# Kernel optimization log

Measured on AMD Instinct MI355X. Metric: run time of the kernel, lower is better.

## Reference

```python
import jax, jax.numpy as jnp
import numpy as np

B, N, K, D, H, FF, L, NH = 8, 50, 20, 3, 128, 2048, 3, 8
S = N * K
HD = H // NH


def setup_inputs() -> dict:
    key = jax.random.key(0)
    ks = jax.random.split(key, 16)
    visited = jax.random.uniform(ks[0], (B, S)) < 0.05
    # the single most-recent action per batch row (status flips 0 -> 1)
    action_idx = jax.random.randint(ks[1], (B,), 0, S)
    visited = visited.at[jnp.arange(B), action_idx].set(True)
    feats = jax.random.normal(ks[2], (B, S, D - 1)) * visited[:, :, None]
    state = jnp.concatenate([feats, visited[:, :, None].astype(jnp.float32)], axis=-1)
    prev_state = state.at[jnp.arange(B), action_idx, :].set(0.0)

    def w(k, shape, s=0.02):
        return jax.random.normal(k, shape, dtype=jnp.float32) * s

    return dict(
        prev_state=prev_state, state=state,
        W_pre=w(ks[3], (D, H)), b_pre=jnp.zeros(H),
        Wq=w(ks[4], (L, H, H)), bq=jnp.zeros((L, H)),
        Wk=w(ks[5], (L, H, H)), bk=jnp.zeros((L, H)),
        Wv=w(ks[6], (L, H, H)), bv=jnp.zeros((L, H)),
        Wo=w(ks[7], (L, H, H)), bo=jnp.zeros((L, H)),
        ln1_g=jnp.ones((L, H)), ln1_b=jnp.zeros((L, H)),
        Wff1=w(ks[8], (L, H, FF)), bff1=jnp.zeros((L, FF)),
        Wff2=w(ks[9], (L, FF, H)), bff2=jnp.zeros((L, H)),
        ln2_g=jnp.ones((L, H)), ln2_b=jnp.zeros((L, H)),
        W_comb=w(ks[10], (2 * H, H)), b_comb=jnp.zeros(H),
        W_dec=w(ks[11], (H, H)), b_dec=jnp.zeros(H),
        W_lin=w(ks[12], (S, S)), b_lin=jnp.zeros(S),
    )


def _layer_norm(x, g, b, eps=1e-5):
    m = jnp.mean(x, -1, keepdims=True)
    v = jnp.mean(jnp.square(x - m), -1, keepdims=True)
    return (x - m) * jax.lax.rsqrt(v + eps) * g + b


def _update_mask(state):
    # vectorized equivalent of the original Python-loop scatter mask
    status = state[:, :, -1] != 0                      # visited [B, S], S = K*N channel-major
    mask = status
    vis_kn = status.reshape(B, K, N)
    user_any = vis_kn.any(axis=1)                      # [B, N]: user visited on any channel
    mask = mask | jnp.broadcast_to(user_any[:, None, :], (B, K, N)).reshape(B, S)
    assigned = state.reshape(B, K, N, D).sum(-1) != 0  # [B, K, N]
    full = assigned.sum(-1) >= 2                       # [B, K]: channel already has 2 users
    mask = mask | jnp.broadcast_to(full[:, :, None], (B, K, N)).reshape(B, S)
    return mask


def reference(prev_state, state, W_pre, b_pre, Wq, bq, Wk, bk, Wv, bv, Wo, bo,
              ln1_g, ln1_b, Wff1, bff1, Wff2, bff2, ln2_g, ln2_b,
              W_comb, b_comb, W_dec, b_dec, W_lin, b_lin):
    mask = _update_mask(state)
    # exactly one status change per batch row (sequential RL step)
    diff = prev_state[:, :, -1] != state[:, :, -1]
    act_idx = jnp.argmax(diff, axis=1)                 # [B]

    x = state @ W_pre + b_pre                          # [B, S, H]
    scale = np.float32(1.0 / np.sqrt(HD))
    for i in range(L):  # 3 post-LN transformer encoder layers
        q = (x @ Wq[i] + bq[i]).reshape(B, S, NH, HD)
        k = (x @ Wk[i] + bk[i]).reshape(B, S, NH, HD)
        v = (x @ Wv[i] + bv[i]).reshape(B, S, NH, HD)
        att = jax.nn.softmax(jnp.einsum('bqhd,bkhd->bhqk', q, k) * scale, axis=-1)
        o = jnp.einsum('bhqk,bkhd->bqhd', att, v).reshape(B, S, H) @ Wo[i] + bo[i]
        x = _layer_norm(x + o, ln1_g[i], ln1_b[i])
        ff = jax.nn.relu(x @ Wff1[i] + bff1[i]) @ Wff2[i] + bff2[i]
        x = _layer_norm(x + ff, ln2_g[i], ln2_b[i])

    last = x[jnp.arange(B), act_idx]                   # [B, H]
    combined = jnp.concatenate([x.mean(axis=1), last], axis=-1)  # [B, 2H]
    g = combined @ W_comb + b_comb                     # [B, H]
    dec = x @ W_dec + b_dec                            # [B, S, H]
    scores = jnp.einsum('bsh,bh->bs', dec, g)          # [B, S]
    masked = scores @ W_lin + b_lin                    # Q-Learning head
    return jnp.where(mask, -jnp.inf, masked)
```

## Files before the change

### kernel.cpp

```cpp
#include <hip/hip_runtime.h>
#include <math.h>

#define Bb 8
#define Ss 1000
#define Kk 20
#define Nn 50
#define Dd 3
#define Hh 128
#define FFf 2048
#define Ll 3
#define NHh 8
#define HDd 16
#define ROWS (Bb*Ss)

#define SENTINEL -3.0e38f

typedef unsigned short ush;
typedef short short8 __attribute__((ext_vector_type(8)));
typedef float f32x4 __attribute__((ext_vector_type(4)));

__device__ __forceinline__ ush f2b(float f) {
  unsigned x = __float_as_uint(f);
  return (ush)((x + 0x7fff + ((x >> 16) & 1)) >> 16);
}

__global__ __launch_bounds__(256) void mask_kernel(const float* __restrict__ state,
                                                   const float* __restrict__ prev_state,
                                                   int* __restrict__ mask, int* __restrict__ act_idx) {
  int b = blockIdx.x, tid = threadIdx.x;
  __shared__ unsigned char status[Ss], assigned[Ss], uany[Nn], fullk[Kk];
  __shared__ int act;
  if (tid == 0) act = 1 << 30;
  __syncthreads();
  for (int s = tid; s < Ss; s += 256) {
    const float* st = state + ((size_t)b * Ss + s) * Dd;
    float f2 = st[2];
    status[s] = (f2 != 0.f);
    assigned[s] = ((st[0] + st[1] + f2) != 0.f);
    float p2 = prev_state[((size_t)b * Ss + s) * Dd + 2];
    if (p2 != f2) atomicMin(&act, s);
  }
  __syncthreads();
  if (tid < Nn) {
    unsigned char a = 0;
    for (int k = 0; k < Kk; ++k) a |= status[k * Nn + tid];
    uany[tid] = a;
  } else if (tid >= 64 && tid < 64 + Kk) {
    int k = tid - 64, cnt = 0;
    for (int n = 0; n < Nn; ++n) cnt += assigned[k * Nn + n];
    fullk[k] = (cnt >= 2);
  }
  __syncthreads();
  for (int s = tid; s < Ss; s += 256)
    mask[b * Ss + s] = (int)(status[s] | uany[s % Nn] | fullk[s / Nn]);
  if (tid == 0) act_idx[b] = (act >= Ss) ? 0 : act;
}

__global__ __launch_bounds__(256) void pre_kernel(const float* __restrict__ state,
                                                  const float* __restrict__ W_pre,
                                                  const float* __restrict__ b_pre,
                                                  float* __restrict__ x, ush* __restrict__ xbf) {
  int idx = blockIdx.x * 256 + threadIdx.x;
  if (idx >= ROWS * Hh) return;
  int row = idx >> 7, n = idx & 127;
  const float* st = state + (size_t)row * Dd;
  float v = b_pre[n] + st[0] * W_pre[n] + st[1] * W_pre[Hh + n] + st[2] * W_pre[2 * Hh + n];
  x[idx] = v;
  xbf[idx] = f2b(v);
}

#define S1 (384*128)
#define S2 (128*128)
#define S3 (2048*128)
#define S4 (128*2048)
#define SPL (S1+S2+S3+S4)
__global__ __launch_bounds__(256) void wprep_kernel(const float* __restrict__ Wq, const float* __restrict__ Wk,
                                                    const float* __restrict__ Wv, const float* __restrict__ Wo,
                                                    const float* __restrict__ Wff1, const float* __restrict__ Wff2,
                                                    const float* __restrict__ bq, const float* __restrict__ bk,
                                                    const float* __restrict__ bv,
                                                    ush* __restrict__ wqkvT, ush* __restrict__ woT,
                                                    ush* __restrict__ wff1T, ush* __restrict__ wff2T,
                                                    float* __restrict__ bqkv) {
  int idx = blockIdx.x * 256 + threadIdx.x;
  if (idx < Ll * SPL) {
    int l = idx / SPL, r = idx % SPL;
    if (r < S1) {
      int k = r / 384, n = r % 384;
      float v = (n < 128) ? Wq[((size_t)l * Hh + k) * Hh + n]
              : (n < 256) ? Wk[((size_t)l * Hh + k) * Hh + (n - 128)]
                          : Wv[((size_t)l * Hh + k) * Hh + (n - 256)];
      wqkvT[((size_t)l * 384 + n) * 128 + k] = f2b(v);
    } else if (r < S1 + S2) {
      int rr = r - S1; int k = rr >> 7, n = rr & 127;
      woT[((size_t)l * 128 + n) * 128 + k] = f2b(Wo[((size_t)l * Hh + k) * Hh + n]);
    } else if (r < S1 + S2 + S3) {
      int rr = r - S1 - S2; int k = rr >> 11, n = rr & 2047;
      wff1T[((size_t)l * 2048 + n) * 128 + k] = f2b(Wff1[((size_t)l * Hh + k) * FFf + n]);
    } else {
      int rr = r - S1 - S2 - S3; int k = rr >> 7, n = rr & 127;
      wff2T[((size_t)l * 128 + n) * 2048 + k] = f2b(Wff2[((size_t)l * FFf + k) * Hh + n]);
    }
  }
  if (idx < Ll * 384) {
    int l = idx / 384, c = idx % 384;
    bqkv[idx] = (c < 128) ? bq[l * Hh + c] : (c < 256 ? bk[l * Hh + c - 128] : bv[l * Hh + c - 256]);
  }
}

#define LDP 40
template <int ABF16, int OBF16, int RELU, int PARTIAL, int QKVV>
__global__ __launch_bounds__(256) void gemm_mfma(const void* __restrict__ A, const ush* __restrict__ Wt,
                                                 const float* __restrict__ bias, void* __restrict__ out,
                                                 int M, int N, int K, int klen, ush* __restrict__ vTout) {
  __shared__ ush As[64 * LDP];
  __shared__ ush Bs[64 * LDP];
  int tid = threadIdx.x;
  int lane = tid & 63, wid = tid >> 6;
  int wr = wid >> 1, wc = wid & 1;
  int m0 = blockIdx.y * 64, n0 = blockIdx.x * 64;
  int lrow = tid >> 2, lk = (tid & 3) << 3;
  int quad = lane >> 4, l16 = lane & 15, kb = quad << 3;
  int kstart = PARTIAL ? blockIdx.z * klen : 0;

  f32x4 acc[2][2];
#pragma unroll
  for (int i = 0; i < 2; ++i)
#pragma unroll
    for (int j = 0; j < 2; ++j) acc[i][j] = (f32x4){0.f, 0.f, 0.f, 0.f};

  for (int k0 = kstart; k0 < kstart + klen; k0 += 32) {
    if (ABF16) {
      short8 av = *(const short8*)((const ush*)A + (size_t)(m0 + lrow) * K + k0 + lk);
      *(short8*)&As[lrow * LDP + lk] = av;
    } else {
      const float* ap = (const float*)A + (size_t)(m0 + lrow) * K + k0 + lk;
      short8 s;
#pragma unroll
      for (int i = 0; i < 8; ++i) s[i] = (short)f2b(ap[i]);
      *(short8*)&As[lrow * LDP + lk] = s;
    }
    short8 bv = *(const short8*)&Wt[(size_t)(n0 + lrow) * K + k0 + lk];
    *(short8*)&Bs[lrow * LDP + lk] = bv;
    __syncthreads();

    short8 a0 = *(short8*)&As[(wr * 32 + l16) * LDP + kb];
    short8 a1 = *(short8*)&As[(wr * 32 + 16 + l16) * LDP + kb];
    short8 b0 = *(short8*)&Bs[(wc * 32 + l16) * LDP + kb];
    short8 b1 = *(short8*)&Bs[(wc * 32 + 16 + l16) * LDP + kb];
    acc[0][0] = __builtin_amdgcn_mfma_f32_16x16x32_bf16(a0, b0, acc[0][0], 0, 0, 0);
    acc[0][1] = __builtin_amdgcn_mfma_f32_16x16x32_bf16(a0, b1, acc[0][1], 0, 0, 0);
    acc[1][0] = __builtin_amdgcn_mfma_f32_16x16x32_bf16(a1, b0, acc[1][0], 0, 0, 0);
    acc[1][1] = __builtin_amdgcn_mfma_f32_16x16x32_bf16(a1, b1, acc[1][1], 0, 0, 0);
    __syncthreads();
  }

  float* pout = PARTIAL ? ((float*)out + (size_t)blockIdx.z * M * N) : (float*)out;
#pragma unroll
  for (int i = 0; i < 2; ++i)
#pragma unroll
    for (int j = 0; j < 2; ++j) {
      int col = n0 + wc * 32 + j * 16 + l16;
      int rbase = m0 + wr * 32 + i * 16 + quad * 4;
      float bval = (!PARTIAL || blockIdx.z == 0) ? bias[col] : 0.f;
#pragma unroll
      for (int v = 0; v < 4; ++v) {
        float o = acc[i][j][v] + bval;
        if (RELU) o = fmaxf(o, 0.f);
        if (QKVV && col >= 256) {
          int row = rbase + v;
          int bb2 = row / 1000, qq = row - bb2 * 1000;
          vTout[((size_t)(bb2 * 128 + (col - 256))) * 1024 + qq] = f2b(o);
        } else if (OBF16) {
          ((ush*)out)[(size_t)(rbase + v) * N + col] = f2b(o);
        } else {
          pout[(size_t)(rbase + v) * N + col] = o;
        }
      }
    }
}

#define WLP 132
__global__ __launch_bounds__(256) void wo_ln_kernel(const ush* __restrict__ A, const ush* __restrict__ Wt,
                                                    const float* __restrict__ bias,
                                                    const float* __restrict__ ln_g, const float* __restrict__ ln_b,
                                                    float* __restrict__ x, ush* __restrict__ xbf) {
  __shared__ char smem[64 * WLP * 4];
  ush* As = (ush*)smem;
  ush* Bs = As + 64 * LDP;
  float* xs = (float*)smem;
  __shared__ float pbias[128], pg[128], pb2[128];

  int tid = threadIdx.x, lane = tid & 63, w = tid >> 6;
  int l16 = lane & 15, quad = lane >> 4, kb = quad * 8;
  int m0 = blockIdx.x * 64;
  if (tid < 128) { pbias[tid] = bias[tid]; pg[tid] = ln_g[tid]; pb2[tid] = ln_b[tid]; }

  f32x4 acc[8];
#pragma unroll
  for (int j = 0; j < 8; ++j) acc[j] = (f32x4){0.f, 0.f, 0.f, 0.f};

  int srow = tid >> 2, slk = (tid & 3) << 3;
  for (int k0 = 0; k0 < 128; k0 += 32) {
    *(short8*)&As[srow * LDP + slk] = *(const short8*)(A + (size_t)(m0 + srow) * 128 + k0 + slk);
#pragma unroll
    for (int rr = 0; rr < 2; ++rr) {
      int row = rr * 64 + srow;
      *(short8*)&Bs[row * LDP + slk] = *(const short8*)(Wt + (size_t)row * 128 + k0 + slk);
    }
    __syncthreads();
    short8 aA = *(short8*)&As[(w * 16 + l16) * LDP + kb];
#pragma unroll
    for (int j = 0; j < 8; ++j) {
      short8 bj = *(short8*)&Bs[(j * 16 + l16) * LDP + kb];
      acc[j] = __builtin_amdgcn_mfma_f32_16x16x32_bf16(aA, bj, acc[j], 0, 0, 0);
    }
    __syncthreads();
  }

  for (int e = tid; e < 64 * 32; e += 256) {
    int idx = e * 4; int row = idx >> 7, col = idx & 127;
    *(float4*)&xs[row * WLP + col] = *(const float4*)&x[(size_t)(m0 + row) * 128 + col];
  }
  __syncthreads();

  float v[8][4], s1[4] = {0.f, 0.f, 0.f, 0.f}, s2[4] = {0.f, 0.f, 0.f, 0.f};
#pragma unroll
  for (int j = 0; j < 8; ++j) {
    int col = j * 16 + l16;
#pragma unroll
    for (int r = 0; r < 4; ++r) {
      int rowt = w * 16 + quad * 4 + r;
      float vv = acc[j][r] + pbias[col] + xs[rowt * WLP + col];
      v[j][r] = vv; s1[r] += vv; s2[r] += vv * vv;
    }
  }
#pragma unroll
  for (int m = 1; m <= 8; m <<= 1) {
#pragma unroll
    for (int r = 0; r < 4; ++r) { s1[r] += __shfl_xor(s1[r], m); s2[r] += __shfl_xor(s2[r], m); }
  }
#pragma unroll
  for (int r = 0; r < 4; ++r) {
    int rowt = w * 16 + quad * 4 + r;
    float mean = s1[r] * (1.f / 128.f);
    float var = s2[r] * (1.f / 128.f) - mean * mean;
    float rstd = rsqrtf(var + 1e-5f);
#pragma unroll
    for (int j = 0; j < 8; ++j) {
      int col = j * 16 + l16;
      float o = (v[j][r] - mean) * rstd * pg[col] + pb2[col];
      size_t gi = (size_t)(m0 + rowt) * 128 + col;
      x[gi] = o; xbf[gi] = f2b(o);
    }
  }
}

#define F2P 72
__global__ __launch_bounds__(256) void ff2_ln_kernel(const ush* __restrict__ A,
                                                     const ush* __restrict__ Wt,
                                                     const float* __restrict__ bias,
                                                     const float* __restrict__ ln_g, const float* __restrict__ ln_b,
                                                     float* __restrict__ x, ush* __restrict__ xbf) {
  __shared__ ush As[32 * F2P];
  __shared__ ush Bs[128 * F2P];
  __shared__ float red1[2][2][16], red2[2][2][16];
  __shared__ float pbias[128], pg[128], pb[128];

  int tid = threadIdx.x, lane = tid & 63, w = tid >> 6;
  int wr = w & 1, wc = w >> 1;
  int l16 = lane & 15, quad = lane >> 4, kb = quad * 8;
  int m0 = blockIdx.x * 32;
  if (tid < 128) { pbias[tid] = bias[tid]; pg[tid] = ln_g[tid]; pb[tid] = ln_b[tid]; }

  f32x4 acc[4];
#pragma unroll
  for (int j = 0; j < 4; ++j) acc[j] = (f32x4){0.f, 0.f, 0.f, 0.f};

  int arow = tid >> 3, alk = (tid & 7) << 3;
  const ush* Ap = A + (size_t)(m0 + arow) * 2048 + alk;

  short8 pa = *(const short8*)Ap;
  short8 pbr[4];
#pragma unroll
  for (int rep = 0; rep < 4; ++rep) {
    int idx = rep * 256 + tid;
    int row = idx >> 3, lk = (idx & 7) << 3;
    pbr[rep] = *(const short8*)(Wt + (size_t)row * 2048 + lk);
  }

  for (int k0 = 0; k0 < 2048; k0 += 64) {
    *(short8*)&As[arow * F2P + alk] = pa;
#pragma unroll
    for (int rep = 0; rep < 4; ++rep) {
      int idx = rep * 256 + tid;
      int row = idx >> 3, lk = (idx & 7) << 3;
      *(short8*)&Bs[row * F2P + lk] = pbr[rep];
    }
    __syncthreads();
    if (k0 + 64 < 2048) {
      pa = *(const short8*)(Ap + k0 + 64);
#pragma unroll
      for (int rep = 0; rep < 4; ++rep) {
        int idx = rep * 256 + tid;
        int row = idx >> 3, lk = (idx & 7) << 3;
        pbr[rep] = *(const short8*)(Wt + (size_t)row * 2048 + k0 + 64 + lk);
      }
    }
#pragma unroll
    for (int kk = 0; kk < 2; ++kk) {
      short8 a = *(short8*)&As[(wr * 16 + l16) * F2P + kk * 32 + kb];
#pragma unroll
      for (int j = 0; j < 4; ++j) {
        short8 b = *(short8*)&Bs[(wc * 64 + j * 16 + l16) * F2P + kk * 32 + kb];
        acc[j] = __builtin_amdgcn_mfma_f32_16x16x32_bf16(a, b, acc[j], 0, 0, 0);
      }
    }
    __syncthreads();
  }

  float v[4][4], s1[4] = {0.f, 0.f, 0.f, 0.f}, s2[4] = {0.f, 0.f, 0.f, 0.f};
#pragma unroll
  for (int j = 0; j < 4; ++j) {
    int col = wc * 64 + j * 16 + l16;
#pragma unroll
    for (int r = 0; r < 4; ++r) {
      int row = m0 + wr * 16 + quad * 4 + r;
      float vv = acc[j][r] + pbias[col] + x[(size_t)row * Hh + col];
      v[j][r] = vv; s1[r] += vv; s2[r] += vv * vv;
    }
  }
#pragma unroll
  for (int m = 1; m <= 8; m <<= 1) {
#pragma unroll
    for (int r = 0; r < 4; ++r) { s1[r] += __shfl_xor(s1[r], m); s2[r] += __shfl_xor(s2[r], m); }
  }
  if (l16 == 0) {
#pragma unroll
    for (int r = 0; r < 4; ++r) {
      red1[wr][wc][quad * 4 + r] = s1[r];
      red2[wr][wc][quad * 4 + r] = s2[r];
    }
  }
  __syncthreads();
#pragma unroll
  for (int r = 0; r < 4; ++r) {
    int qr = quad * 4 + r;
    float t1 = red1[wr][0][qr] + red1[wr][1][qr];
    float t2 = red2[wr][0][qr] + red2[wr][1][qr];
    float mean = t1 * (1.f / 128.f);
    float var = t2 * (1.f / 128.f) - mean * mean;
    float rstd = rsqrtf(var + 1e-5f);
    int row = m0 + wr * 16 + quad * 4 + r;
#pragma unroll
    for (int j = 0; j < 4; ++j) {
      int col = wc * 64 + j * 16 + l16;
      float o = (v[j][r] - mean) * rstd * pg[col] + pb[col];
      size_t gi = (size_t)row * Hh + col;
      x[gi] = o; xbf[gi] = f2b(o);
    }
  }
}

__global__ __launch_bounds__(256) void attn_mfma(const ush* __restrict__ qkv,
                                                 const ush* __restrict__ vT,
                                                 ush* __restrict__ attn_o) {
  int blk = blockIdx.x;
  int local = blk >> 3;
  int bh = ((blk & 7) << 3) | (local >> 4);
  int qt = local & 15;
  int b = bh >> 3, h = bh & 7;
  int qbase = qt * 64;
  int tid = threadIdx.x, lane = tid & 63, w = tid >> 6;
  int l16 = lane & 15, quad = lane >> 4, kb = quad * 8;

  __shared__ ush Ks[2][64][40];
  __shared__ ush Vs[2][16][72];
  __shared__ ush Pb[4][16][72];

  if (tid < 128) {
    int row = tid >> 1, g = tid & 1;
    *(short8*)&Ks[0][row][16 + g * 8] = (short8){0, 0, 0, 0, 0, 0, 0, 0};
    *(short8*)&Ks[1][row][16 + g * 8] = (short8){0, 0, 0, 0, 0, 0, 0, 0};
  }

  int qrow = qbase + w * 16 + l16; if (qrow >= Ss) qrow = Ss - 1;
  short8 aq = *(const short8*)(qkv + (size_t)(b * Ss + qrow) * 384 + h * HDd + kb);

  int srow = tid >> 1, sg = tid & 1;
  int sd = (tid - 128) >> 3, skg = (tid - 128) & 7;
  const ush* kbase = qkv + (size_t)b * Ss * 384 + 128 + h * HDd;
  const ush* vbase = vT + (size_t)(b * 128 + h * 16) * 1024;

  if (tid < 128) {
    short8 s8 = (short8){0, 0, 0, 0, 0, 0, 0, 0};
    if (srow < Ss) s8 = *(const short8*)(kbase + (size_t)srow * 384 + sg * 8);
    *(short8*)&Ks[0][srow][sg * 8] = s8;
  } else {
    *(short8*)&Vs[0][sd][skg * 8] = *(const short8*)(vbase + (size_t)sd * 1024 + skg * 8);
  }
  __syncthreads();

  const short one_b = (short)0x3F80;
  const short8 ones = (short8){one_b, one_b, one_b, one_b, one_b, one_b, one_b, one_b};
  f32x4 acc_pv = (f32x4){0.f, 0.f, 0.f, 0.f};
  f32x4 acc_l = (f32x4){0.f, 0.f, 0.f, 0.f};
  const f32x4 zero4 = (f32x4){0.f, 0.f, 0.f, 0.f};

  for (int it = 0; it < 16; ++it) {
    int k0 = it * 64;
    int cur = it & 1, nxt = cur ^ 1;
    bool have = (it + 1 < 16);

    short8 gk, gv;
    if (have) {
      if (tid < 128) {
        gk = (short8){0, 0, 0, 0, 0, 0, 0, 0};
        int key = k0 + 64 + srow;
        if (key < Ss) gk = *(const short8*)(kbase + (size_t)key * 384 + sg * 8);
      } else {
        gv = *(const short8*)(vbase + (size_t)sd * 1024 + k0 + 64 + skg * 8);
      }
    }

    bool tail = (k0 + 64 > Ss);
#pragma unroll
    for (int kn = 0; kn < 4; ++kn) {
      short8 ak = *(short8*)&Ks[cur][kn * 16 + l16][kb];
      f32x4 s = __builtin_amdgcn_mfma_f32_16x16x32_bf16(ak, aq, zero4, 0, 0, 0);
      float p0 = __expf(s[0] * 0.25f);
      float p1 = __expf(s[1] * 0.25f);
      float p2 = __expf(s[2] * 0.25f);
      float p3 = __expf(s[3] * 0.25f);
      if (tail) {
        int keyb = k0 + kn * 16 + quad * 4;
        if (keyb + 0 >= Ss) p0 = 0.f;
        if (keyb + 1 >= Ss) p1 = 0.f;
        if (keyb + 2 >= Ss) p2 = 0.f;
        if (keyb + 3 >= Ss) p3 = 0.f;
      }
      unsigned lo, hi;
      asm("v_cvt_pk_bf16_f32 %0, %1, %2" : "=v"(lo) : "v"(p0), "v"(p1));
      asm("v_cvt_pk_bf16_f32 %0, %1, %2" : "=v"(hi) : "v"(p2), "v"(p3));
      *(uint2*)&Pb[w][l16][kn * 16 + quad * 4] = make_uint2(lo, hi);
    }

    short8 pa0 = *(short8*)&Pb[w][l16][kb];
    short8 pa1 = *(short8*)&Pb[w][l16][32 + kb];
    short8 vb0 = *(short8*)&Vs[cur][l16][kb];
    short8 vb1 = *(short8*)&Vs[cur][l16][32 + kb];
    acc_pv = __builtin_amdgcn_mfma_f32_16x16x32_bf16(pa0, vb0, acc_pv, 0, 0, 0);
    acc_pv = __builtin_amdgcn_mfma_f32_16x16x32_bf16(pa1, vb1, acc_pv, 0, 0, 0);
    acc_l = __builtin_amdgcn_mfma_f32_16x16x32_bf16(pa0, ones, acc_l, 0, 0, 0);
    acc_l = __builtin_amdgcn_mfma_f32_16x16x32_bf16(pa1, ones, acc_l, 0, 0, 0);

    if (have) {
      if (tid < 128) *(short8*)&Ks[nxt][srow][sg * 8] = gk;
      else *(short8*)&Vs[nxt][sd][skg * 8] = gv;
    }
    __syncthreads();
  }

#pragma unroll
  for (int r = 0; r < 4; ++r) {
    int q = qbase + w * 16 + quad * 4 + r;
    if (q < Ss)
      attn_o[((size_t)(b * Ss + q)) * Hh + h * HDd + l16] = f2b(acc_pv[r] / acc_l[r]);
  }
}

__global__ __launch_bounds__(128) void mean_part_kernel(const float* __restrict__ x,
                                                        float* __restrict__ mpart) {
  int c = blockIdx.x, b = blockIdx.y, n = threadIdx.x;
  const float* xb = x + ((size_t)b * Ss + c * 125) * Hh + n;
  float s = 0.f;
#pragma unroll 5
  for (int i = 0; i < 125; ++i) s += xb[(size_t)i * Hh];
  mpart[(c * Bb + b) * Hh + n] = s;
}

__global__ __launch_bounds__(128) void ghc_kernel(const float* __restrict__ x, const float* __restrict__ mpart,
                                                  const int* __restrict__ act_idx,
                                                  const float* __restrict__ W_comb, const float* __restrict__ b_comb,
                                                  const float* __restrict__ W_dec, const float* __restrict__ b_dec,
                                                  float* __restrict__ h, float* __restrict__ cb) {
  int b = blockIdx.x, n = threadIdx.x;
  __shared__ float cs[2 * Hh], gs[Hh], red[2];
  float mean = 0.f;
#pragma unroll
  for (int c = 0; c < 8; ++c) mean += mpart[(c * Bb + b) * Hh + n];
  cs[n] = mean * (1.f / Ss);
  cs[Hh + n] = x[((size_t)b * Ss + act_idx[b]) * Hh + n];
  __syncthreads();
  float acc = b_comb[n];
  for (int j = 0; j < 2 * Hh; ++j) acc += cs[j] * W_comb[(size_t)j * Hh + n];
  gs[n] = acc;
  __syncthreads();
  float hv = 0.f;
  for (int c = 0; c < Hh; ++c) hv += W_dec[(size_t)n * Hh + c] * gs[c];
  h[b * Hh + n] = hv;
  float t = b_dec[n] * gs[n];
  for (int off = 32; off; off >>= 1) t += __shfl_down(t, off);
  if ((n & 63) == 0) red[n >> 6] = t;
  __syncthreads();
  if (n == 0) cb[b] = red[0] + red[1];
}

__global__ __launch_bounds__(256) void scores_kernel(const float* __restrict__ x, const float* __restrict__ h,
                                                     const float* __restrict__ cb, float* __restrict__ scores) {
  int wid = threadIdx.x >> 6, lane = threadIdx.x & 63;
  int row = blockIdx.x * 4 + wid;
  if (row >= ROWS) return;
  int b = row / Ss;
  const float* xr = x + (size_t)row * Hh;
  const float* hb = h + b * Hh;
  float s = xr[lane] * hb[lane] + xr[lane + 64] * hb[lane + 64];
  for (int off = 32; off; off >>= 1) s += __shfl_down(s, off);
  if (lane == 0) scores[row] = s + cb[b];
}

__global__ __launch_bounds__(256) void final_part(const float* __restrict__ scores,
                                                  const float* __restrict__ W_lin,
                                                  float* __restrict__ fpart) {
  int spc = blockIdx.x, kc = blockIdx.y;
  int tid = threadIdx.x;
  __shared__ float ss[8][125];
  for (int i = tid; i < 8 * 125; i += 256) {
    int bb = i / 125, s = i - bb * 125;
    ss[bb][s] = scores[bb * Ss + kc * 125 + s];
  }
  __syncthreads();
  if (tid < 250) {
    int sp = spc * 250 + tid;
    float acc[8];
#pragma unroll
    for (int bb = 0; bb < 8; ++bb) acc[bb] = 0.f;
    const float* wl = &W_lin[(size_t)(kc * 125) * Ss + sp];
#pragma unroll 5
    for (int s = 0; s < 125; ++s) {
      float wv = wl[(size_t)s * Ss];
#pragma unroll
      for (int bb = 0; bb < 8; ++bb) acc[bb] = fmaf(ss[bb][s], wv, acc[bb]);
    }
#pragma unroll
    for (int bb = 0; bb < 8; ++bb)
      fpart[((size_t)kc * Bb + bb) * Ss + sp] = acc[bb];
  }
}

__global__ __launch_bounds__(256) void final_combine(const float* __restrict__ fpart,
                                                     const float* __restrict__ b_lin,
                                                     const int* __restrict__ mask,
                                                     float* __restrict__ out) {
  int b = blockIdx.y;
  int sp = blockIdx.x * 256 + threadIdx.x;
  if (sp >= Ss) return;
  float acc = b_lin[sp];
#pragma unroll
  for (int kc = 0; kc < 8; ++kc) acc += fpart[((size_t)kc * Bb + b) * Ss + sp];
  out[b * Ss + sp] = mask[b * Ss + sp] ? SENTINEL : acc;
}

extern "C" void kernel_launch(void* const* d_in, const int* in_sizes, int n_in,
                              void* d_out, int out_size, void* d_ws, size_t ws_size,
                              hipStream_t stream) {
  const float* prev_state = (const float*)d_in[0];
  const float* state = (const float*)d_in[1];
  const float* W_pre = (const float*)d_in[2];
  const float* b_pre = (const float*)d_in[3];
  const float* Wq = (const float*)d_in[4];
  const float* bq = (const float*)d_in[5];
  const float* Wk = (const float*)d_in[6];
  const float* bk = (const float*)d_in[7];
  const float* Wv = (const float*)d_in[8];
  const float* bv = (const float*)d_in[9];
  const float* Wo = (const float*)d_in[10];
  const float* bo = (const float*)d_in[11];
  const float* ln1_g = (const float*)d_in[12];
  const float* ln1_b = (const float*)d_in[13];
  const float* Wff1 = (const float*)d_in[14];
  const float* bff1 = (const float*)d_in[15];
  const float* Wff2 = (const float*)d_in[16];
  const float* bff2 = (const float*)d_in[17];
  const float* ln2_g = (const float*)d_in[18];
  const float* ln2_b = (const float*)d_in[19];
  const float* W_comb = (const float*)d_in[20];
  const float* b_comb = (const float*)d_in[21];
  const float* W_dec = (const float*)d_in[22];
  const float* b_dec = (const float*)d_in[23];
  const float* W_lin = (const float*)d_in[24];
  const float* b_lin = (const float*)d_in[25];

  char* wsp = (char*)d_ws;
  auto alloc = [&](size_t bytes) { char* p = wsp; wsp += (bytes + 255) & ~(size_t)255; return p; };
  int* mask = (int*)alloc(ROWS * 4);
  int* act = (int*)alloc(Bb * 4);
  ush* wqkvT = (ush*)alloc((size_t)Ll * 384 * 128 * 2);
  ush* woT = (ush*)alloc((size_t)Ll * 128 * 128 * 2);
  ush* wff1T = (ush*)alloc((size_t)Ll * 2048 * 128 * 2);
  ush* wff2T = (ush*)alloc((size_t)Ll * 128 * 2048 * 2);
  float* bqkv = (float*)alloc((size_t)Ll * 384 * 4);
  float* x = (float*)alloc((size_t)ROWS * Hh * 4);
  ush* xbf = (ush*)alloc((size_t)ROWS * Hh * 2);
  ush* qkv_bf = (ush*)alloc((size_t)ROWS * 384 * 2);
  ush* vT = (ush*)alloc((size_t)Bb * 128 * 1024 * 2);
  ush* attn_ob = (ush*)alloc((size_t)ROWS * Hh * 2);
  float* mpart = (float*)alloc((size_t)8 * Bb * Hh * 4);
  float* hbuf = (float*)alloc((size_t)Bb * Hh * 4);
  float* cb = (float*)alloc((size_t)Bb * 4);
  float* scores = (float*)alloc((size_t)ROWS * 4);
  float* fpart = (float*)alloc((size_t)8 * Bb * Ss * 4);
  ush* ffb = (ush*)alloc((size_t)ROWS * FFf * 2);

  wprep_kernel<<<dim3((Ll * SPL + 255) / 256), 256, 0, stream>>>(Wq, Wk, Wv, Wo, Wff1, Wff2, bq, bk, bv,
                                                                 wqkvT, woT, wff1T, wff2T, bqkv);
  mask_kernel<<<Bb, 256, 0, stream>>>(state, prev_state, mask, act);
  pre_kernel<<<dim3((ROWS * Hh + 255) / 256), 256, 0, stream>>>(state, W_pre, b_pre, x, xbf);

  for (int l = 0; l < Ll; ++l) {
    gemm_mfma<1, 1, 0, 0, 1><<<dim3(384 / 64, ROWS / 64), 256, 0, stream>>>(
        xbf, wqkvT + (size_t)l * 384 * 128, bqkv + l * 384, qkv_bf, ROWS, 384, 128, 128, vT);
    attn_mfma<<<dim3(1024), 256, 0, stream>>>(qkv_bf, vT, attn_ob);
    wo_ln_kernel<<<dim3(ROWS / 64), 256, 0, stream>>>(
        attn_ob, woT + (size_t)l * 128 * 128, bo + l * Hh, ln1_g + l * Hh, ln1_b + l * Hh, x, xbf);
    gemm_mfma<1, 1, 1, 0, 0><<<dim3(2048 / 64, ROWS / 64), 256, 0, stream>>>(
        xbf, wff1T + (size_t)l * 2048 * 128, bff1 + l * FFf, ffb, ROWS, 2048, 128, 128, nullptr);
    ff2_ln_kernel<<<dim3(ROWS / 32), 256, 0, stream>>>(
        ffb, wff2T + (size_t)l * 128 * 2048, bff2 + l * Hh, ln2_g + l * Hh, ln2_b + l * Hh, x, xbf);
  }

  mean_part_kernel<<<dim3(8, Bb), 128, 0, stream>>>(x, mpart);
  ghc_kernel<<<Bb, 128, 0, stream>>>(x, mpart, act, W_comb, b_comb, W_dec, b_dec, hbuf, cb);
  scores_kernel<<<dim3(ROWS / 4), 256, 0, stream>>>(x, hbuf, cb, scores);
  final_part<<<dim3(4, 8), 256, 0, stream>>>(scores, W_lin, fpart);
  final_combine<<<dim3(4, Bb), 256, 0, stream>>>(fpart, b_lin, mask, (float*)d_out);
}
```

Baseline: 385.6 us.

## Double-buffer LDS in GEMM kernels and unify Wo/FF2 LayerNorm GEMMs

The generic MFMA GEMM now uses two LDS buffers, prefetching the next K-tile into registers during the MFMA work and storing it to the other buffer, which removes one barrier per iteration. The separate Wo+LN kernel is replaced by a templated version of the FF2+LN kernel (32-row tiles, double-buffered) that also serves K=128, giving more blocks for the Wo projection. W_dec is transposed during weight prep so the ghc kernel reads it coalesced. The costs are twice the LDS per block, which may limit occupancy, and a Wo path that now shares the FF2 kernel's tile shape.

```diff
diff --git a/kernel.cpp b/kernel.cpp
--- a/kernel.cpp
+++ b/kernel.cpp
@@ -78,10 +78,10 @@
                                                     const float* __restrict__ Wv, const float* __restrict__ Wo,
                                                     const float* __restrict__ Wff1, const float* __restrict__ Wff2,
                                                     const float* __restrict__ bq, const float* __restrict__ bk,
-                                                    const float* __restrict__ bv,
+                                                    const float* __restrict__ bv, const float* __restrict__ W_dec,
                                                     ush* __restrict__ wqkvT, ush* __restrict__ woT,
                                                     ush* __restrict__ wff1T, ush* __restrict__ wff2T,
-                                                    float* __restrict__ bqkv) {
+                                                    float* __restrict__ bqkv, float* __restrict__ wdecT) {
   int idx = blockIdx.x * 256 + threadIdx.x;
   if (idx < Ll * SPL) {
     int l = idx / SPL, r = idx % SPL;
@@ -106,22 +106,28 @@
     int l = idx / 384, c = idx % 384;
     bqkv[idx] = (c < 128) ? bq[l * Hh + c] : (c < 256 ? bk[l * Hh + c - 128] : bv[l * Hh + c - 256]);
   }
+  if (idx < Hh * Hh) {
+    int k = idx >> 7, n = idx & 127;
+    wdecT[(size_t)n * Hh + k] = W_dec[idx];
+  }
 }
 
 #define LDP 40
-template <int ABF16, int OBF16, int RELU, int PARTIAL, int QKVV>
-__global__ __launch_bounds__(256) void gemm_mfma(const void* __restrict__ A, const ush* __restrict__ Wt,
-                                                 const float* __restrict__ bias, void* __restrict__ out,
-                                                 int M, int N, int K, int klen, ush* __restrict__ vTout) {
-  __shared__ ush As[64 * LDP];
-  __shared__ ush Bs[64 * LDP];
+template <int RELU, int QKVV>
+__global__ __launch_bounds__(256) void gemm_mfma(const ush* __restrict__ A, const ush* __restrict__ Wt,
+                                                 const float* __restrict__ bias, ush* __restrict__ out,
+                                                 int N, int K, ush* __restrict__ vTout) {
+  __shared__ ush As[2][64 * LDP];
+  __shared__ ush Bs[2][64 * LDP];
   int tid = threadIdx.x;
   int lane = tid & 63, wid = tid >> 6;
   int wr = wid >> 1, wc = wid & 1;
   int m0 = blockIdx.y * 64, n0 = blockIdx.x * 64;
   int lrow = tid >> 2, lk = (tid & 3) << 3;
   int quad = lane >> 4, l16 = lane & 15, kb = quad << 3;
-  int kstart = PARTIAL ? blockIdx.z * klen : 0;
+
+  const ush* Ap = A + (size_t)(m0 + lrow) * K + lk;
+  const ush* Bp = Wt + (size_t)(n0 + lrow) * K + lk;
 
   f32x4 acc[2][2];
 #pragma unroll
@@ -129,40 +135,42 @@
 #pragma unroll
     for (int j = 0; j < 2; ++j) acc[i][j] = (f32x4){0.f, 0.f, 0.f, 0.f};
 
-  for (int k0 = kstart; k0 < kstart + klen; k0 += 32) {
-    if (ABF16) {
-      short8 av = *(const short8*)((const ush*)A + (size_t)(m0 + lrow) * K + k0 + lk);
-      *(short8*)&As[lrow * LDP + lk] = av;
-    } else {
-      const float* ap = (const float*)A + (size_t)(m0 + lrow) * K + k0 + lk;
-      short8 s;
-#pragma unroll
-      for (int i = 0; i < 8; ++i) s[i] = (short)f2b(ap[i]);
-      *(short8*)&As[lrow * LDP + lk] = s;
-    }
-    short8 bv = *(const short8*)&Wt[(size_t)(n0 + lrow) * K + k0 + lk];
-    *(short8*)&Bs[lrow * LDP + lk] = bv;
-    __syncthreads();
-
-    short8 a0 = *(short8*)&As[(wr * 32 + l16) * LDP + kb];
-    short8 a1 = *(short8*)&As[(wr * 32 + 16 + l16) * LDP + kb];
-    short8 b0 = *(short8*)&Bs[(wc * 32 + l16) * LDP + kb];
-    short8 b1 = *(short8*)&Bs[(wc * 32 + 16 + l16) * LDP + kb];
+  short8 pa = *(const short8*)Ap;
+  short8 pb = *(const short8*)Bp;
+  *(short8*)&As[0][lrow * LDP + lk] = pa;
+  *(short8*)&Bs[0][lrow * LDP + lk] = pb;
+  __syncthreads();
+
+  int NT = K >> 5;
+  for (int it = 0; it < NT; ++it) {
+    int cur = it & 1;
+    bool have = (it + 1 < NT);
+    if (have) {
+      pa = *(const short8*)(Ap + (it + 1) * 32);
+      pb = *(const short8*)(Bp + (it + 1) * 32);
+    }
+    short8 a0 = *(short8*)&As[cur][(wr * 32 + l16) * LDP + kb];
+    short8 a1 = *(short8*)&As[cur][(wr * 32 + 16 + l16) * LDP + kb];
+    short8 b0 = *(short8*)&Bs[cur][(wc * 32 + l16) * LDP + kb];
+    short8 b1 = *(short8*)&Bs[cur][(wc * 32 + 16 + l16) * LDP + kb];
     acc[0][0] = __builtin_amdgcn_mfma_f32_16x16x32_bf16(a0, b0, acc[0][0], 0, 0, 0);
     acc[0][1] = __builtin_amdgcn_mfma_f32_16x16x32_bf16(a0, b1, acc[0][1], 0, 0, 0);
     acc[1][0] = __builtin_amdgcn_mfma_f32_16x16x32_bf16(a1, b0, acc[1][0], 0, 0, 0);
     acc[1][1] = __builtin_amdgcn_mfma_f32_16x16x32_bf16(a1, b1, acc[1][1], 0, 0, 0);
+    if (have) {
+      *(short8*)&As[cur ^ 1][lrow * LDP + lk] = pa;
+      *(short8*)&Bs[cur ^ 1][lrow * LDP + lk] = pb;
+    }
     __syncthreads();
   }
 
-  float* pout = PARTIAL ? ((float*)out + (size_t)blockIdx.z * M * N) : (float*)out;
 #pragma unroll
   for (int i = 0; i < 2; ++i)
 #pragma unroll
     for (int j = 0; j < 2; ++j) {
       int col = n0 + wc * 32 + j * 16 + l16;
       int rbase = m0 + wr * 32 + i * 16 + quad * 4;
-      float bval = (!PARTIAL || blockIdx.z == 0) ? bias[col] : 0.f;
+      float bval = bias[col];
 #pragma unroll
       for (int v = 0; v < 4; ++v) {
         float o = acc[i][j][v] + bval;
@@ -171,99 +179,22 @@
           int row = rbase + v;
           int bb2 = row / 1000, qq = row - bb2 * 1000;
           vTout[((size_t)(bb2 * 128 + (col - 256))) * 1024 + qq] = f2b(o);
-        } else if (OBF16) {
-          ((ush*)out)[(size_t)(rbase + v) * N + col] = f2b(o);
         } else {
-          pout[(size_t)(rbase + v) * N + col] = o;
+          out[(size_t)(rbase + v) * N + col] = f2b(o);
         }
       }
     }
 }
 
-#define WLP 132
-__global__ __launch_bounds__(256) void wo_ln_kernel(const ush* __restrict__ A, const ush* __restrict__ Wt,
-                                                    const float* __restrict__ bias,
-                                                    const float* __restrict__ ln_g, const float* __restrict__ ln_b,
-                                                    float* __restrict__ x, ush* __restrict__ xbf) {
-  __shared__ char smem[64 * WLP * 4];
-  ush* As = (ush*)smem;
-  ush* Bs = As + 64 * LDP;
-  float* xs = (float*)smem;
-  __shared__ float pbias[128], pg[128], pb2[128];
-
-  int tid = threadIdx.x, lane = tid & 63, w = tid >> 6;
-  int l16 = lane & 15, quad = lane >> 4, kb = quad * 8;
-  int m0 = blockIdx.x * 64;
-  if (tid < 128) { pbias[tid] = bias[tid]; pg[tid] = ln_g[tid]; pb2[tid] = ln_b[tid]; }
-
-  f32x4 acc[8];
-#pragma unroll
-  for (int j = 0; j < 8; ++j) acc[j] = (f32x4){0.f, 0.f, 0.f, 0.f};
-
-  int srow = tid >> 2, slk = (tid & 3) << 3;
-  for (int k0 = 0; k0 < 128; k0 += 32) {
-    *(short8*)&As[srow * LDP + slk] = *(const short8*)(A + (size_t)(m0 + srow) * 128 + k0 + slk);
-#pragma unroll
-    for (int rr = 0; rr < 2; ++rr) {
-      int row = rr * 64 + srow;
-      *(short8*)&Bs[row * LDP + slk] = *(const short8*)(Wt + (size_t)row * 128 + k0 + slk);
-    }
-    __syncthreads();
-    short8 aA = *(short8*)&As[(w * 16 + l16) * LDP + kb];
-#pragma unroll
-    for (int j = 0; j < 8; ++j) {
-      short8 bj = *(short8*)&Bs[(j * 16 + l16) * LDP + kb];
-      acc[j] = __builtin_amdgcn_mfma_f32_16x16x32_bf16(aA, bj, acc[j], 0, 0, 0);
-    }
-    __syncthreads();
-  }
-
-  for (int e = tid; e < 64 * 32; e += 256) {
-    int idx = e * 4; int row = idx >> 7, col = idx & 127;
-    *(float4*)&xs[row * WLP + col] = *(const float4*)&x[(size_t)(m0 + row) * 128 + col];
-  }
-  __syncthreads();
-
-  float v[8][4], s1[4] = {0.f, 0.f, 0.f, 0.f}, s2[4] = {0.f, 0.f, 0.f, 0.f};
-#pragma unroll
-  for (int j = 0; j < 8; ++j) {
-    int col = j * 16 + l16;
-#pragma unroll
-    for (int r = 0; r < 4; ++r) {
-      int rowt = w * 16 + quad * 4 + r;
-      float vv = acc[j][r] + pbias[col] + xs[rowt * WLP + col];
-      v[j][r] = vv; s1[r] += vv; s2[r] += vv * vv;
-    }
-  }
-#pragma unroll
-  for (int m = 1; m <= 8; m <<= 1) {
-#pragma unroll
-    for (int r = 0; r < 4; ++r) { s1[r] += __shfl_xor(s1[r], m); s2[r] += __shfl_xor(s2[r], m); }
-  }
-#pragma unroll
-  for (int r = 0; r < 4; ++r) {
-    int rowt = w * 16 + quad * 4 + r;
-    float mean = s1[r] * (1.f / 128.f);
-    float var = s2[r] * (1.f / 128.f) - mean * mean;
-    float rstd = rsqrtf(var + 1e-5f);
-#pragma unroll
-    for (int j = 0; j < 8; ++j) {
-      int col = j * 16 + l16;
-      float o = (v[j][r] - mean) * rstd * pg[col] + pb2[col];
-      size_t gi = (size_t)(m0 + rowt) * 128 + col;
-      x[gi] = o; xbf[gi] = f2b(o);
-    }
-  }
-}
-
 #define F2P 72
-__global__ __launch_bounds__(256) void ff2_ln_kernel(const ush* __restrict__ A,
-                                                     const ush* __restrict__ Wt,
-                                                     const float* __restrict__ bias,
-                                                     const float* __restrict__ ln_g, const float* __restrict__ ln_b,
-                                                     float* __restrict__ x, ush* __restrict__ xbf) {
-  __shared__ ush As[32 * F2P];
-  __shared__ ush Bs[128 * F2P];
+template <int KK>
+__global__ __launch_bounds__(256) void gemm_ln_kernel(const ush* __restrict__ A,
+                                                      const ush* __restrict__ Wt,
+                                                      const float* __restrict__ bias,
+                                                      const float* __restrict__ ln_g, const float* __restrict__ ln_b,
+                                                      float* __restrict__ x, ush* __restrict__ xbf) {
+  __shared__ ush As[2][32 * F2P];
+  __shared__ ush Bs[2][128 * F2P];
   __shared__ float red1[2][2][16], red2[2][2][16];
   __shared__ float pbias[128], pg[128], pb[128];
 
@@ -278,43 +209,44 @@
   for (int j = 0; j < 4; ++j) acc[j] = (f32x4){0.f, 0.f, 0.f, 0.f};
 
   int arow = tid >> 3, alk = (tid & 7) << 3;
-  const ush* Ap = A + (size_t)(m0 + arow) * 2048 + alk;
+  const ush* Ap = A + (size_t)(m0 + arow) * KK + alk;
+  const ush* Bp = Wt + (size_t)arow * KK + alk;
 
   short8 pa = *(const short8*)Ap;
   short8 pbr[4];
 #pragma unroll
-  for (int rep = 0; rep < 4; ++rep) {
-    int idx = rep * 256 + tid;
-    int row = idx >> 3, lk = (idx & 7) << 3;
-    pbr[rep] = *(const short8*)(Wt + (size_t)row * 2048 + lk);
-  }
-
-  for (int k0 = 0; k0 < 2048; k0 += 64) {
-    *(short8*)&As[arow * F2P + alk] = pa;
-#pragma unroll
-    for (int rep = 0; rep < 4; ++rep) {
-      int idx = rep * 256 + tid;
-      int row = idx >> 3, lk = (idx & 7) << 3;
-      *(short8*)&Bs[row * F2P + lk] = pbr[rep];
-    }
-    __syncthreads();
-    if (k0 + 64 < 2048) {
-      pa = *(const short8*)(Ap + k0 + 64);
-#pragma unroll
-      for (int rep = 0; rep < 4; ++rep) {
-        int idx = rep * 256 + tid;
-        int row = idx >> 3, lk = (idx & 7) << 3;
-        pbr[rep] = *(const short8*)(Wt + (size_t)row * 2048 + k0 + 64 + lk);
-      }
+  for (int rep = 0; rep < 4; ++rep)
+    pbr[rep] = *(const short8*)(Bp + (size_t)rep * 32 * KK);
+  *(short8*)&As[0][arow * F2P + alk] = pa;
+#pragma unroll
+  for (int rep = 0; rep < 4; ++rep)
+    *(short8*)&Bs[0][(rep * 32 + arow) * F2P + alk] = pbr[rep];
+  __syncthreads();
+
+  const int NT = KK / 64;
+  for (int it = 0; it < NT; ++it) {
+    int cur = it & 1;
+    bool have = (it + 1 < NT);
+    if (have) {
+      pa = *(const short8*)(Ap + (it + 1) * 64);
+#pragma unroll
+      for (int rep = 0; rep < 4; ++rep)
+        pbr[rep] = *(const short8*)(Bp + (size_t)rep * 32 * KK + (it + 1) * 64);
     }
 #pragma unroll
     for (int kk = 0; kk < 2; ++kk) {
-      short8 a = *(short8*)&As[(wr * 16 + l16) * F2P + kk * 32 + kb];
+      short8 a = *(short8*)&As[cur][(wr * 16 + l16) * F2P + kk * 32 + kb];
 #pragma unroll
       for (int j = 0; j < 4; ++j) {
-        short8 b = *(short8*)&Bs[(wc * 64 + j * 16 + l16) * F2P + kk * 32 + kb];
+        short8 b = *(short8*)&Bs[cur][(wc * 64 + j * 16 + l16) * F2P + kk * 32 + kb];
         acc[j] = __builtin_amdgcn_mfma_f32_16x16x32_bf16(a, b, acc[j], 0, 0, 0);
       }
+    }
+    if (have) {
+      *(short8*)&As[cur ^ 1][arow * F2P + alk] = pa;
+#pragma unroll
+      for (int rep = 0; rep < 4; ++rep)
+        *(short8*)&Bs[cur ^ 1][(rep * 32 + arow) * F2P + alk] = pbr[rep];
     }
     __syncthreads();
   }
@@ -482,7 +414,7 @@
 __global__ __launch_bounds__(128) void ghc_kernel(const float* __restrict__ x, const float* __restrict__ mpart,
                                                   const int* __restrict__ act_idx,
                                                   const float* __restrict__ W_comb, const float* __restrict__ b_comb,
-                                                  const float* __restrict__ W_dec, const float* __restrict__ b_dec,
+                                                  const float* __restrict__ wdecT, const float* __restrict__ b_dec,
                                                   float* __restrict__ h, float* __restrict__ cb) {
   int b = blockIdx.x, n = threadIdx.x;
   __shared__ float cs[2 * Hh], gs[Hh], red[2];
@@ -497,7 +429,7 @@
   gs[n] = acc;
   __syncthreads();
   float hv = 0.f;
-  for (int c = 0; c < Hh; ++c) hv += W_dec[(size_t)n * Hh + c] * gs[c];
+  for (int c = 0; c < Hh; ++c) hv += wdecT[(size_t)c * Hh + n] * gs[c];
   h[b * Hh + n] = hv;
   float t = b_dec[n] * gs[n];
   for (int off = 32; off; off >>= 1) t += __shfl_down(t, off);
@@ -600,6 +532,7 @@
   ush* wff1T = (ush*)alloc((size_t)Ll * 2048 * 128 * 2);
   ush* wff2T = (ush*)alloc((size_t)Ll * 128 * 2048 * 2);
   float* bqkv = (float*)alloc((size_t)Ll * 384 * 4);
+  float* wdecT = (float*)alloc((size_t)Hh * Hh * 4);
   float* x = (float*)alloc((size_t)ROWS * Hh * 4);
   ush* xbf = (ush*)alloc((size_t)ROWS * Hh * 2);
   ush* qkv_bf = (ush*)alloc((size_t)ROWS * 384 * 2);
@@ -612,25 +545,25 @@
   float* fpart = (float*)alloc((size_t)8 * Bb * Ss * 4);
   ush* ffb = (ush*)alloc((size_t)ROWS * FFf * 2);
 
-  wprep_kernel<<<dim3((Ll * SPL + 255) / 256), 256, 0, stream>>>(Wq, Wk, Wv, Wo, Wff1, Wff2, bq, bk, bv,
-                                                                 wqkvT, woT, wff1T, wff2T, bqkv);
+  wprep_kernel<<<dim3((Ll * SPL + 255) / 256), 256, 0, stream>>>(Wq, Wk, Wv, Wo, Wff1, Wff2, bq, bk, bv, W_dec,
+                                                                 wqkvT, woT, wff1T, wff2T, bqkv, wdecT);
   mask_kernel<<<Bb, 256, 0, stream>>>(state, prev_state, mask, act);
   pre_kernel<<<dim3((ROWS * Hh + 255) / 256), 256, 0, stream>>>(state, W_pre, b_pre, x, xbf);
 
   for (int l = 0; l < Ll; ++l) {
-    gemm_mfma<1, 1, 0, 0, 1><<<dim3(384 / 64, ROWS / 64), 256, 0, stream>>>(
-        xbf, wqkvT + (size_t)l * 384 * 128, bqkv + l * 384, qkv_bf, ROWS, 384, 128, 128, vT);
+    gemm_mfma<0, 1><<<dim3(384 / 64, ROWS / 64), 256, 0, stream>>>(
+        xbf, wqkvT + (size_t)l * 384 * 128, bqkv + l * 384, qkv_bf, 384, 128, vT);
     attn_mfma<<<dim3(1024), 256, 0, stream>>>(qkv_bf, vT, attn_ob);
-    wo_ln_kernel<<<dim3(ROWS / 64), 256, 0, stream>>>(
+    gemm_ln_kernel<128><<<dim3(ROWS / 32), 256, 0, stream>>>(
         attn_ob, woT + (size_t)l * 128 * 128, bo + l * Hh, ln1_g + l * Hh, ln1_b + l * Hh, x, xbf);
-    gemm_mfma<1, 1, 1, 0, 0><<<dim3(2048 / 64, ROWS / 64), 256, 0, stream>>>(
-        xbf, wff1T + (size_t)l * 2048 * 128, bff1 + l * FFf, ffb, ROWS, 2048, 128, 128, nullptr);
-    ff2_ln_kernel<<<dim3(ROWS / 32), 256, 0, stream>>>(
+    gemm_mfma<1, 0><<<dim3(2048 / 64, ROWS / 64), 256, 0, stream>>>(
+        xbf, wff1T + (size_t)l * 2048 * 128, bff1 + l * FFf, ffb, 2048, 128, nullptr);
+    gemm_ln_kernel<2048><<<dim3(ROWS / 32), 256, 0, stream>>>(
         ffb, wff2T + (size_t)l * 128 * 2048, bff2 + l * Hh, ln2_g + l * Hh, ln2_b + l * Hh, x, xbf);
   }
 
   mean_part_kernel<<<dim3(8, Bb), 128, 0, stream>>>(x, mpart);
-  ghc_kernel<<<Bb, 128, 0, stream>>>(x, mpart, act, W_comb, b_comb, W_dec, b_dec, hbuf, cb);
+  ghc_kernel<<<Bb, 128, 0, stream>>>(x, mpart, act, W_comb, b_comb, wdecT, b_dec, hbuf, cb);
   scores_kernel<<<dim3(ROWS / 4), 256, 0, stream>>>(x, hbuf, cb, scores);
   final_part<<<dim3(4, 8), 256, 0, stream>>>(scores, W_lin, fpart);
   final_combine<<<dim3(4, Bb), 256, 0, stream>>>(fpart, b_lin, mask, (float*)d_out);
```

Measured after the change: 381.2 us. About the same (-1.2%).
